# Kernel tuning notes

Measured on AMD Instinct MI355X. Metric: run time of the kernel, lower is better.

## Reference

```python
import jax, jax.numpy as jnp
import numpy as np

N, E, C, H, M = 10000, 160000, 512, 512, 2000  # nodes, edges, in=out ch, hidden ch, missing nodes


def setup_inputs() -> dict:
    key = jax.random.key(0)
    ks = jax.random.split(key, 9)
    s = 0.05  # weight init scale
    x = jax.random.normal(ks[0], (N, C), dtype=jnp.float32)
    edge_index = jax.random.randint(ks[1], (2, E), 0, N, dtype=jnp.int32)
    W1 = jax.random.normal(ks[2], (C, H), dtype=jnp.float32) * s
    b1 = jnp.zeros((H,), dtype=jnp.float32)
    W2 = jax.random.normal(ks[3], (H, H), dtype=jnp.float32) * s
    b2 = jnp.zeros((H,), dtype=jnp.float32)
    W3 = jax.random.normal(ks[4], (H, C), dtype=jnp.float32) * s
    b3 = jnp.zeros((C,), dtype=jnp.float32)
    noise = jax.random.normal(ks[5], (M, H), dtype=jnp.float32)  # stands in for torch.randn in forward
    return {"x": x, "edge_index": edge_index, "W1": W1, "b1": b1, "W2": W2,
            "b2": b2, "W3": W3, "b3": b3, "noise": noise, "num_missing_nodes": M}


def reference(x, edge_index, W1, b1, W2, b2, W3, b3, noise, num_missing_nodes):
    n = x.shape[0]
    loops = jnp.arange(n, dtype=edge_index.dtype)
    src = jnp.concatenate([edge_index[0], loops])  # add self-loops (PyG GCNConv default)
    dst = jnp.concatenate([edge_index[1], loops])
    deg = jax.ops.segment_sum(jnp.ones_like(dst, x.dtype), dst, num_segments=n)
    dis = jnp.where(deg > 0, jax.lax.rsqrt(jnp.maximum(deg, 1.0)), 0.0)
    norm = dis[src] * dis[dst]  # [E+N]

    def gcn(h, W, b):
        h = h @ W                              # linear (no bias) before aggregation
        msg = norm[:, None] * h[src]           # gather + normalize
        return jax.ops.segment_sum(msg, dst, num_segments=n) + b  # scatter-add + bias

    h = jax.nn.relu(gcn(x, W1, b1))
    h = jax.nn.relu(gcn(h, W2, b2))
    pred = noise @ W3 + b3                     # [M, C]
    return jnp.concatenate([h, pred], axis=0)  # [N+M, C] (requires H == C)
```

## Files before the change

kernel.cpp:

```cpp
#include <hip/hip_runtime.h>
#include <hip/hip_bf16.h>

typedef __attribute__((ext_vector_type(8))) short short8;
typedef __attribute__((ext_vector_type(8))) unsigned short ushort8v;
typedef __attribute__((ext_vector_type(4))) float f32x4;

#define CDIM 512
#define SLOTS 64

__device__ __forceinline__ float bf2f(unsigned short u) {
    union { unsigned int i; float f; } w; w.i = ((unsigned int)u) << 16; return w.f;
}
__device__ __forceinline__ unsigned short f2bf(float f) {
    __bf16 b = (__bf16)f;
    union { __bf16 b; unsigned short u; } w; w.b = b;
    return w.u;
}

__device__ __forceinline__ void decode_bxby(int b, int nbA, int& bx, int& by) {
    int nfull = (nbA >> 3) << 5;
    if (b < nfull) {
        int sup = b >> 5, loc = b & 31;
        bx = sup * 8 + (loc & 7);
        by = loc >> 3;
    } else {
        int bb = b - nfull;
        bx = ((nbA >> 3) << 3) + (bb >> 2);
        by = bb & 3;
    }
}

__global__ __launch_bounds__(256) void prep_kernel(
    const float* __restrict__ W1, const float* __restrict__ W2,
    const float* __restrict__ W3,
    unsigned short* __restrict__ W1t, unsigned short* __restrict__ W2t,
    unsigned short* __restrict__ W3t,
    int* __restrict__ cz, int n2) {
    int b = blockIdx.x;
    if (b < 192) {
        int w = b >> 6;
        const float* s = (w == 0) ? W1 : (w == 1) ? W2 : W3;
        unsigned short* d = (w == 0) ? W1t : (w == 1) ? W2t : W3t;
        int tb = b & 63;
        int k0 = (tb >> 3) << 6, n0 = (tb & 7) << 6;
        __shared__ unsigned short ld[64][66];
        int t = threadIdx.x;
        {
            int kk = t >> 2, nseg = (t & 3) * 16;
            const float4* sp = (const float4*)(s + (size_t)(k0 + kk) * 512 + n0 + nseg);
            float4 f0 = sp[0], f1 = sp[1], f2 = sp[2], f3 = sp[3];
            unsigned short* lp = &ld[kk][nseg];
            lp[0] = f2bf(f0.x);  lp[1] = f2bf(f0.y);  lp[2] = f2bf(f0.z);  lp[3] = f2bf(f0.w);
            lp[4] = f2bf(f1.x);  lp[5] = f2bf(f1.y);  lp[6] = f2bf(f1.z);  lp[7] = f2bf(f1.w);
            lp[8] = f2bf(f2.x);  lp[9] = f2bf(f2.y);  lp[10] = f2bf(f2.z); lp[11] = f2bf(f2.w);
            lp[12] = f2bf(f3.x); lp[13] = f2bf(f3.y); lp[14] = f2bf(f3.z); lp[15] = f2bf(f3.w);
        }
        __syncthreads();
        {
            int nn = t >> 2, kseg = (t & 3) * 16;
            ushort8v o0, o1;
#pragma unroll
            for (int i = 0; i < 8; i++) { o0[i] = ld[kseg + i][nn]; o1[i] = ld[kseg + 8 + i][nn]; }
            unsigned short* dp = d + (size_t)(n0 + nn) * 512 + k0 + kseg;
            *(ushort8v*)(dp) = o0;
            *(ushort8v*)(dp + 8) = o1;
        }
    } else {
        int i = (b - 192) * 256 + threadIdx.x;
        if (i < n2) cz[i] = 0;
    }
}

__global__ void count_kernel(const int* __restrict__ dst, int* __restrict__ counts, int E) {
    int i4 = (blockIdx.x * blockDim.x + threadIdx.x) * 4;
    if (i4 + 4 <= E) {
        int4 d = *(const int4*)(dst + i4);
        atomicAdd(&counts[d.x], 1);
        atomicAdd(&counts[d.y], 1);
        atomicAdd(&counts[d.z], 1);
        atomicAdd(&counts[d.w], 1);
    } else {
        for (int j = i4; j < E; j++) atomicAdd(&counts[dst[j]], 1);
    }
}

template <int AF32, int MODE>
__device__ __forceinline__ void gemm_block64(
    const float* __restrict__ Af, const unsigned short* __restrict__ Ab,
    const unsigned short* __restrict__ Bt, const float* __restrict__ bias,
    const int* __restrict__ cnt,
    unsigned short* __restrict__ outb, float* __restrict__ outf,
    int Mrows, int bx, int by)
{
    const int K = 512;
    __shared__ unsigned short As[64][72];
    __shared__ unsigned short Bs[128][72];

    int t = threadIdx.x;
    int lane = t & 63;
    int wid = t >> 6;
    int wm = wid >> 1, wn = wid & 1;
    int m0 = bx * 64;
    int n0 = by * 128;

    f32x4 acc[2][4];
#pragma unroll
    for (int i = 0; i < 2; i++)
#pragma unroll
        for (int j = 0; j < 4; j++) acc[i][j] = (f32x4){0.f, 0.f, 0.f, 0.f};

    int arow = t >> 2;
    int aseg = (t & 3) * 16;
    int brow = t >> 1;
    int bseg = (t & 1) * 32;
    int agr = m0 + arow;
    bool aok = (agr < Mrows);

    ushort8v ra[2];
    ushort8v rb[4];

    auto loadA = [&](int k0) {
        if (aok) {
            if (AF32) {
                const float4* ap = (const float4*)(Af + (size_t)agr * K + k0 + aseg);
                float4 f0 = ap[0], f1 = ap[1], f2 = ap[2], f3 = ap[3];
                ra[0][0] = f2bf(f0.x); ra[0][1] = f2bf(f0.y); ra[0][2] = f2bf(f0.z); ra[0][3] = f2bf(f0.w);
                ra[0][4] = f2bf(f1.x); ra[0][5] = f2bf(f1.y); ra[0][6] = f2bf(f1.z); ra[0][7] = f2bf(f1.w);
                ra[1][0] = f2bf(f2.x); ra[1][1] = f2bf(f2.y); ra[1][2] = f2bf(f2.z); ra[1][3] = f2bf(f2.w);
                ra[1][4] = f2bf(f3.x); ra[1][5] = f2bf(f3.y); ra[1][6] = f2bf(f3.z); ra[1][7] = f2bf(f3.w);
            } else {
                const ushort8v* ap = (const ushort8v*)(Ab + (size_t)agr * K + k0 + aseg);
                ra[0] = ap[0]; ra[1] = ap[1];
            }
        } else {
            ushort8v z = (ushort8v){0,0,0,0,0,0,0,0};
            ra[0] = z; ra[1] = z;
        }
    };
    auto loadB = [&](int k0) {
        const ushort8v* bp = (const ushort8v*)(Bt + (size_t)(n0 + brow) * K + k0 + bseg);
        rb[0] = bp[0]; rb[1] = bp[1]; rb[2] = bp[2]; rb[3] = bp[3];
    };
    auto storeAB = [&]() {
        *(ushort8v*)&As[arow][aseg + 0] = ra[0];
        *(ushort8v*)&As[arow][aseg + 8] = ra[1];
        *(ushort8v*)&Bs[brow][bseg + 0]  = rb[0];
        *(ushort8v*)&Bs[brow][bseg + 8]  = rb[1];
        *(ushort8v*)&Bs[brow][bseg + 16] = rb[2];
        *(ushort8v*)&Bs[brow][bseg + 24] = rb[3];
    };

    loadA(0); loadB(0); storeAB();
    __syncthreads();

    for (int k0 = 0; k0 < K; k0 += 64) {
        bool more = (k0 + 64 < K);
        if (more) { loadA(k0 + 64); loadB(k0 + 64); }

#pragma unroll
        for (int ks = 0; ks < 64; ks += 32) {
            short8 af[2], bf[4];
            int kk = ks + 8 * (lane >> 4);
            int rbase = wm * 32 + (lane & 15);
            int cbase = wn * 64 + (lane & 15);
#pragma unroll
            for (int fm = 0; fm < 2; fm++) af[fm] = *(const short8*)&As[rbase + fm * 16][kk];
#pragma unroll
            for (int fn = 0; fn < 4; fn++) bf[fn] = *(const short8*)&Bs[cbase + fn * 16][kk];
#pragma unroll
            for (int fm = 0; fm < 2; fm++)
#pragma unroll
                for (int fn = 0; fn < 4; fn++)
                    acc[fm][fn] = __builtin_amdgcn_mfma_f32_16x16x32_bf16(af[fm], bf[fn], acc[fm][fn], 0, 0, 0);
        }
        __syncthreads();
        if (more) {
            storeAB();
            __syncthreads();
        }
    }

    int rl = (lane >> 4) * 4;
    int cc = lane & 15;
#pragma unroll
    for (int fm = 0; fm < 2; fm++) {
#pragma unroll
        for (int r = 0; r < 4; r++) {
            int row = m0 + wm * 32 + fm * 16 + rl + r;
            if (row >= Mrows) continue;
            float dv = (MODE == 2) ? rsqrtf((float)(cnt[row] + 1)) : 0.f;
#pragma unroll
            for (int fn = 0; fn < 4; fn++) {
                int col = n0 + wn * 64 + fn * 16 + cc;
                float v = acc[fm][fn][r];
                if (MODE == 1)
                    outf[(size_t)row * CDIM + col] = v + bias[col];
                else
                    outb[(size_t)row * CDIM + col] = f2bf(dv * v);
            }
        }
    }
}

__global__ __launch_bounds__(256) void gemm1_pred_fill_kernel(
    const float* __restrict__ x, const unsigned short* __restrict__ W1t,
    const int* __restrict__ counts, unsigned short* __restrict__ t0,
    const float* __restrict__ noise, const unsigned short* __restrict__ W3t,
    const float* __restrict__ b3, float* __restrict__ out_pred,
    const int* __restrict__ esrc, const int* __restrict__ edst,
    int* __restrict__ cursor, int* __restrict__ cols,
    int N, int M, int E, int nbA, int nbP)
{
    int b = blockIdx.x;
    int nbG = nbA * 4, nbP4 = nbP * 4;
    if (b < nbG) {
        int bx, by; decode_bxby(b, nbA, bx, by);
        gemm_block64<1, 2>(x, nullptr, W1t, nullptr, counts, t0, nullptr, N, bx, by);
    } else if (b < nbG + nbP4) {
        int bx, by; decode_bxby(b - nbG, nbP, bx, by);
        gemm_block64<1, 1>(noise, nullptr, W3t, b3, nullptr, nullptr, out_pred, M, bx, by);
    } else {
        int i = (b - nbG - nbP4) * 256 + threadIdx.x;
        if (i < E) {
            int d = edst[i];
            int pos = atomicAdd(&cursor[d], 1);
            if (pos < SLOTS) cols[(d << 6) + pos] = esrc[i];
        }
    }
}

__global__ __launch_bounds__(256) void gemm2_kernel(
    const unsigned short* __restrict__ h1, const unsigned short* __restrict__ W2t,
    const int* __restrict__ counts, unsigned short* __restrict__ t1, int N, int nbA)
{
    int bx, by; decode_bxby(blockIdx.x, nbA, bx, by);
    gemm_block64<0, 2>(nullptr, h1, W2t, nullptr, counts, t1, nullptr, N, bx, by);
}

template <int OUTF32>
__global__ __launch_bounds__(256) void aggregate_kernel(
    const unsigned short* __restrict__ t,
    const int* __restrict__ counts, const int* __restrict__ cols,
    const float* __restrict__ bias,
    unsigned short* __restrict__ outb, float* __restrict__ outf, int n)
{
    int gw = (blockIdx.x * 256 + threadIdx.x) >> 6;
    if (gw >= n) return;
    int lane = threadIdx.x & 63;
    int cbase = lane * 8;

    int deg = min(counts[gw], SLOTS);
    float di = rsqrtf((float)(counts[gw] + 1));
    ushort8v v = *(const ushort8v*)(t + (size_t)gw * CDIM + cbase);
    float acc[8];
#pragma unroll
    for (int j = 0; j < 8; j++) acc[j] = bf2f(v[j]);

    const int* cp = cols + ((size_t)gw << 6);
    int s = 0;
    for (; s + 4 <= deg; s += 4) {
        int s0 = cp[s], s1 = cp[s + 1], s2 = cp[s + 2], s3 = cp[s + 3];
        ushort8v u0 = *(const ushort8v*)(t + (size_t)s0 * CDIM + cbase);
        ushort8v u1 = *(const ushort8v*)(t + (size_t)s1 * CDIM + cbase);
        ushort8v u2 = *(const ushort8v*)(t + (size_t)s2 * CDIM + cbase);
        ushort8v u3 = *(const ushort8v*)(t + (size_t)s3 * CDIM + cbase);
#pragma unroll
        for (int j = 0; j < 8; j++)
            acc[j] += (bf2f(u0[j]) + bf2f(u1[j])) + (bf2f(u2[j]) + bf2f(u3[j]));
    }
    for (; s < deg; ++s) {
        int src = cp[s];
        ushort8v u = *(const ushort8v*)(t + (size_t)src * CDIM + cbase);
#pragma unroll
        for (int j = 0; j < 8; j++) acc[j] += bf2f(u[j]);
    }

    if (OUTF32) {
        float4 o0, o1;
        o0.x = fmaxf(di * acc[0] + bias[cbase + 0], 0.f);
        o0.y = fmaxf(di * acc[1] + bias[cbase + 1], 0.f);
        o0.z = fmaxf(di * acc[2] + bias[cbase + 2], 0.f);
        o0.w = fmaxf(di * acc[3] + bias[cbase + 3], 0.f);
        o1.x = fmaxf(di * acc[4] + bias[cbase + 4], 0.f);
        o1.y = fmaxf(di * acc[5] + bias[cbase + 5], 0.f);
        o1.z = fmaxf(di * acc[6] + bias[cbase + 6], 0.f);
        o1.w = fmaxf(di * acc[7] + bias[cbase + 7], 0.f);
        *(float4*)(outf + (size_t)gw * CDIM + cbase) = o0;
        *(float4*)(outf + (size_t)gw * CDIM + cbase + 4) = o1;
    } else {
        ushort8v o;
#pragma unroll
        for (int j = 0; j < 8; j++) {
            float t2 = fmaxf(di * acc[j] + bias[cbase + j], 0.f);
            o[j] = f2bf(t2);
        }
        *(ushort8v*)(outb + (size_t)gw * CDIM + cbase) = o;
    }
}

extern "C" void kernel_launch(void* const* d_in, const int* in_sizes, int n_in,
                              void* d_out, int out_size, void* d_ws, size_t ws_size,
                              hipStream_t stream) {
    const float* x     = (const float*)d_in[0];
    const int*   ei    = (const int*)d_in[1];
    const float* W1    = (const float*)d_in[2];
    const float* b1    = (const float*)d_in[3];
    const float* W2    = (const float*)d_in[4];
    const float* b2    = (const float*)d_in[5];
    const float* W3    = (const float*)d_in[6];
    const float* b3    = (const float*)d_in[7];
    const float* noise = (const float*)d_in[8];

    const int N = in_sizes[0] / CDIM;
    const int E = in_sizes[1] / 2;
    const int M = in_sizes[8] / CDIM;
    const int* esrc = ei;
    const int* edst = ei + E;

    char* ws = (char*)d_ws;
    size_t off = 0;
    auto alloc = [&](size_t bytes) -> void* {
        void* p = ws + off;
        off += (bytes + 255) & ~(size_t)255;
        return p;
    };
    unsigned short* W1t = (unsigned short*)alloc(512 * 512 * 2);
    unsigned short* W2t = (unsigned short*)alloc(512 * 512 * 2);
    unsigned short* W3t = (unsigned short*)alloc(512 * 512 * 2);
    unsigned short* t0  = (unsigned short*)alloc((size_t)N * CDIM * 2);
    unsigned short* h1b = (unsigned short*)alloc((size_t)N * CDIM * 2);
    int*   cz   = (int*)alloc((size_t)2 * N * 4);
    int*   cols = (int*)alloc((size_t)N * SLOTS * 4);
    int* counts = cz;
    int* cursor = cz + N;

    float* out_h    = (float*)d_out;
    float* out_pred = (float*)d_out + (size_t)N * CDIM;

    const int nbA = (N + 63) / 64;
    const int nbP = (M + 63) / 64;
    const int ZB  = (2 * N + 255) / 256;
    const int FB  = (E + 255) / 256;
    const int nbG = nbA * 4, nbP4 = nbP * 4;

    prep_kernel<<<192 + ZB, 256, 0, stream>>>(W1, W2, W3, W1t, W2t, W3t, cz, 2 * N);
    count_kernel<<<(E / 4 + 255) / 256, 256, 0, stream>>>(edst, counts, E);
    gemm1_pred_fill_kernel<<<nbG + nbP4 + FB, 256, 0, stream>>>(
        x, W1t, counts, t0, noise, W3t, b3, out_pred, esrc, edst, cursor, cols,
        N, M, E, nbA, nbP);
    int agg_blocks = (N + 3) / 4;
    aggregate_kernel<0><<<agg_blocks, 256, 0, stream>>>(t0, counts, cols, b1, h1b, nullptr, N);
    gemm2_kernel<<<nbG, 256, 0, stream>>>(h1b, W2t, counts, t0, N, nbA);
    aggregate_kernel<1><<<agg_blocks, 256, 0, stream>>>(t0, counts, cols, b2, nullptr, out_h, N);
}
```

Before: 111.6 us.

## Drop separate degree-count kernel by reusing fill cursor as degree

Removes the count_kernel pass over edges and uses the cursor from the CSR fill as the in-degree. Since degrees are not known during GEMM1, the first layer's source normalization moves into the first aggregation, which reads the degree of each neighbour and multiplies per edge. The fp32 output stores also switch to nontemporal stores. This saves one launch and one atomic pass, but adds scattered degree loads and per-edge rsqrt in the first aggregation.

```diff
diff --git a/kernel.cpp b/kernel.cpp
--- a/kernel.cpp
+++ b/kernel.cpp
@@ -35,7 +35,7 @@
     const float* __restrict__ W3,
     unsigned short* __restrict__ W1t, unsigned short* __restrict__ W2t,
     unsigned short* __restrict__ W3t,
-    int* __restrict__ cz, int n2) {
+    int* __restrict__ cursor, int n) {
     int b = blockIdx.x;
     if (b < 192) {
         int w = b >> 6;
@@ -67,20 +67,7 @@
         }
     } else {
         int i = (b - 192) * 256 + threadIdx.x;
-        if (i < n2) cz[i] = 0;
-    }
-}
-
-__global__ void count_kernel(const int* __restrict__ dst, int* __restrict__ counts, int E) {
-    int i4 = (blockIdx.x * blockDim.x + threadIdx.x) * 4;
-    if (i4 + 4 <= E) {
-        int4 d = *(const int4*)(dst + i4);
-        atomicAdd(&counts[d.x], 1);
-        atomicAdd(&counts[d.y], 1);
-        atomicAdd(&counts[d.z], 1);
-        atomicAdd(&counts[d.w], 1);
-    } else {
-        for (int j = i4; j < E; j++) atomicAdd(&counts[dst[j]], 1);
+        if (i < n) cursor[i] = 0;
     }
 }
 
@@ -188,15 +175,18 @@
         for (int r = 0; r < 4; r++) {
             int row = m0 + wm * 32 + fm * 16 + rl + r;
             if (row >= Mrows) continue;
-            float dv = (MODE == 2) ? rsqrtf((float)(cnt[row] + 1)) : 0.f;
+            float dv = (MODE == 2) ? rsqrtf((float)(cnt[row] + 1)) : 1.f;
 #pragma unroll
             for (int fn = 0; fn < 4; fn++) {
                 int col = n0 + wn * 64 + fn * 16 + cc;
                 float v = acc[fm][fn][r];
-                if (MODE == 1)
-                    outf[(size_t)row * CDIM + col] = v + bias[col];
-                else
+                if (MODE == 1) {
+                    __builtin_nontemporal_store(v + bias[col], outf + (size_t)row * CDIM + col);
+                } else if (MODE == 2) {
                     outb[(size_t)row * CDIM + col] = f2bf(dv * v);
+                } else {
+                    outb[(size_t)row * CDIM + col] = f2bf(v);
+                }
             }
         }
     }
@@ -204,7 +194,7 @@
 
 __global__ __launch_bounds__(256) void gemm1_pred_fill_kernel(
     const float* __restrict__ x, const unsigned short* __restrict__ W1t,
-    const int* __restrict__ counts, unsigned short* __restrict__ t0,
+    unsigned short* __restrict__ t0,
     const float* __restrict__ noise, const unsigned short* __restrict__ W3t,
     const float* __restrict__ b3, float* __restrict__ out_pred,
     const int* __restrict__ esrc, const int* __restrict__ edst,
@@ -215,7 +205,7 @@
     int nbG = nbA * 4, nbP4 = nbP * 4;
     if (b < nbG) {
         int bx, by; decode_bxby(b, nbA, bx, by);
-        gemm_block64<1, 2>(x, nullptr, W1t, nullptr, counts, t0, nullptr, N, bx, by);
+        gemm_block64<1, 3>(x, nullptr, W1t, nullptr, nullptr, t0, nullptr, N, bx, by);
     } else if (b < nbG + nbP4) {
         int bx, by; decode_bxby(b - nbG, nbP, bx, by);
         gemm_block64<1, 1>(noise, nullptr, W3t, b3, nullptr, nullptr, out_pred, M, bx, by);
@@ -237,7 +227,7 @@
     gemm_block64<0, 2>(nullptr, h1, W2t, nullptr, counts, t1, nullptr, N, bx, by);
 }
 
-template <int OUTF32>
+template <int SRCW, int OUTF32>
 __global__ __launch_bounds__(256) void aggregate_kernel(
     const unsigned short* __restrict__ t,
     const int* __restrict__ counts, const int* __restrict__ cols,
@@ -253,40 +243,46 @@
     float di = rsqrtf((float)(counts[gw] + 1));
     ushort8v v = *(const ushort8v*)(t + (size_t)gw * CDIM + cbase);
     float acc[8];
-#pragma unroll
-    for (int j = 0; j < 8; j++) acc[j] = bf2f(v[j]);
+    float selfw = SRCW ? di : 1.f;
+#pragma unroll
+    for (int j = 0; j < 8; j++) acc[j] = selfw * bf2f(v[j]);
 
     const int* cp = cols + ((size_t)gw << 6);
     int s = 0;
     for (; s + 4 <= deg; s += 4) {
         int s0 = cp[s], s1 = cp[s + 1], s2 = cp[s + 2], s3 = cp[s + 3];
+        float w0 = 1.f, w1 = 1.f, w2 = 1.f, w3 = 1.f;
+        if (SRCW) {
+            w0 = rsqrtf((float)(counts[s0] + 1));
+            w1 = rsqrtf((float)(counts[s1] + 1));
+            w2 = rsqrtf((float)(counts[s2] + 1));
+            w3 = rsqrtf((float)(counts[s3] + 1));
+        }
         ushort8v u0 = *(const ushort8v*)(t + (size_t)s0 * CDIM + cbase);
         ushort8v u1 = *(const ushort8v*)(t + (size_t)s1 * CDIM + cbase);
         ushort8v u2 = *(const ushort8v*)(t + (size_t)s2 * CDIM + cbase);
         ushort8v u3 = *(const ushort8v*)(t + (size_t)s3 * CDIM + cbase);
 #pragma unroll
-        for (int j = 0; j < 8; j++)
-            acc[j] += (bf2f(u0[j]) + bf2f(u1[j])) + (bf2f(u2[j]) + bf2f(u3[j]));
+        for (int j = 0; j < 8; j++) {
+            if (SRCW)
+                acc[j] += (w0 * bf2f(u0[j]) + w1 * bf2f(u1[j])) + (w2 * bf2f(u2[j]) + w3 * bf2f(u3[j]));
+            else
+                acc[j] += (bf2f(u0[j]) + bf2f(u1[j])) + (bf2f(u2[j]) + bf2f(u3[j]));
+        }
     }
     for (; s < deg; ++s) {
         int src = cp[s];
+        float w = SRCW ? rsqrtf((float)(counts[src] + 1)) : 1.f;
         ushort8v u = *(const ushort8v*)(t + (size_t)src * CDIM + cbase);
 #pragma unroll
-        for (int j = 0; j < 8; j++) acc[j] += bf2f(u[j]);
+        for (int j = 0; j < 8; j++) acc[j] += w * bf2f(u[j]);
     }
 
     if (OUTF32) {
-        float4 o0, o1;
-        o0.x = fmaxf(di * acc[0] + bias[cbase + 0], 0.f);
-        o0.y = fmaxf(di * acc[1] + bias[cbase + 1], 0.f);
-        o0.z = fmaxf(di * acc[2] + bias[cbase + 2], 0.f);
-        o0.w = fmaxf(di * acc[3] + bias[cbase + 3], 0.f);
-        o1.x = fmaxf(di * acc[4] + bias[cbase + 4], 0.f);
-        o1.y = fmaxf(di * acc[5] + bias[cbase + 5], 0.f);
-        o1.z = fmaxf(di * acc[6] + bias[cbase + 6], 0.f);
-        o1.w = fmaxf(di * acc[7] + bias[cbase + 7], 0.f);
-        *(float4*)(outf + (size_t)gw * CDIM + cbase) = o0;
-        *(float4*)(outf + (size_t)gw * CDIM + cbase + 4) = o1;
+        float* op = outf + (size_t)gw * CDIM + cbase;
+#pragma unroll
+        for (int j = 0; j < 8; j++)
+            __builtin_nontemporal_store(fmaxf(di * acc[j] + bias[cbase + j], 0.f), op + j);
     } else {
         ushort8v o;
 #pragma unroll
@@ -329,27 +325,24 @@
     unsigned short* W3t = (unsigned short*)alloc(512 * 512 * 2);
     unsigned short* t0  = (unsigned short*)alloc((size_t)N * CDIM * 2);
     unsigned short* h1b = (unsigned short*)alloc((size_t)N * CDIM * 2);
-    int*   cz   = (int*)alloc((size_t)2 * N * 4);
-    int*   cols = (int*)alloc((size_t)N * SLOTS * 4);
-    int* counts = cz;
-    int* cursor = cz + N;
+    int*   cursor = (int*)alloc((size_t)N * 4);
+    int*   cols   = (int*)alloc((size_t)N * SLOTS * 4);
 
     float* out_h    = (float*)d_out;
     float* out_pred = (float*)d_out + (size_t)N * CDIM;
 
     const int nbA = (N + 63) / 64;
     const int nbP = (M + 63) / 64;
-    const int ZB  = (2 * N + 255) / 256;
+    const int ZB  = (N + 255) / 256;
     const int FB  = (E + 255) / 256;
     const int nbG = nbA * 4, nbP4 = nbP * 4;
 
-    prep_kernel<<<192 + ZB, 256, 0, stream>>>(W1, W2, W3, W1t, W2t, W3t, cz, 2 * N);
-    count_kernel<<<(E / 4 + 255) / 256, 256, 0, stream>>>(edst, counts, E);
+    prep_kernel<<<192 + ZB, 256, 0, stream>>>(W1, W2, W3, W1t, W2t, W3t, cursor, N);
     gemm1_pred_fill_kernel<<<nbG + nbP4 + FB, 256, 0, stream>>>(
-        x, W1t, counts, t0, noise, W3t, b3, out_pred, esrc, edst, cursor, cols,
+        x, W1t, t0, noise, W3t, b3, out_pred, esrc, edst, cursor, cols,
         N, M, E, nbA, nbP);
     int agg_blocks = (N + 3) / 4;
-    aggregate_kernel<0><<<agg_blocks, 256, 0, stream>>>(t0, counts, cols, b1, h1b, nullptr, N);
-    gemm2_kernel<<<nbG, 256, 0, stream>>>(h1b, W2t, counts, t0, N, nbA);
-    aggregate_kernel<1><<<agg_blocks, 256, 0, stream>>>(t0, counts, cols, b2, nullptr, out_h, N);
-}
+    aggregate_kernel<1, 0><<<agg_blocks, 256, 0, stream>>>(t0, cursor, cols, b1, h1b, nullptr, N);
+    gemm2_kernel<<<nbG, 256, 0, stream>>>(h1b, W2t, cursor, t0, N, nbA);
+    aggregate_kernel<0, 1><<<agg_blocks, 256, 0, stream>>>(t0, cursor, cols, b2, nullptr, out_h, N);
+}
```

Result: faster. 99.27 us (-11.1%).
